# Kernel tuning notes

Hardware: AMD Instinct MI355X
Metric: run time of the kernel (lower is better)

## Reference

```python
import jax, jax.numpy as jnp
import numpy as np

CHAR_SIZE = 155   # len of the module's char_list
B, S, C, D = 64, 128, 16, 256


def setup_inputs() -> dict:
    key = jax.random.key(0)
    k1, k2, k3, k4 = jax.random.split(key, 4)
    x = jax.random.randint(k1, (B, S, C), 0, CHAR_SIZE)
    emb = jax.random.normal(k2, (CHAR_SIZE, D), dtype=jnp.float32) * 0.05
    W = jax.random.normal(k3, (D, 4 * D), dtype=jnp.float32) * 0.05
    U = jax.random.normal(k4, (D, 4 * D), dtype=jnp.float32) * 0.05
    b = jnp.zeros((4 * D,), dtype=jnp.float32)
    return {"x": x, "emb": emb, "W": W, "U": U, "b": b}


def reference(x, emb, W, U, b):
    b_, s_, c_ = x.shape
    d = emb.shape[1]
    e = emb[x]                                   # (B, S, C, D) embedding lookup
    xs = e.reshape(b_ * s_, c_, d)               # (B*S, C, D)
    # precompute input contributions for all timesteps (one big GEMM)
    xz = jnp.einsum('btd,de->bte', xs, W) + b    # (B*S, C, 4D)

    def step(carry, z_x):
        h, c = carry
        z = z_x + h @ U                          # (B*S, 4D)
        zi, zf, zg, zo = jnp.split(z, 4, axis=-1)  # Keras gate order i,f,c,o
        i = jax.nn.sigmoid(zi)
        f = jax.nn.sigmoid(zf)
        o = jax.nn.sigmoid(zo)
        c = f * c + i * zg                       # activation=None -> identity candidate
        h = o * c                                # activation=None -> identity output
        return (h, c), None

    h0 = jnp.zeros((b_ * s_, d), dtype=xz.dtype)
    (h, _), _ = jax.lax.scan(step, (h0, h0), jnp.swapaxes(xz, 0, 1))
    return h.reshape(b_, s_, d)                  # (B, S, D)
```

## Files before the change

### kernel.cpp

```cpp
#include <hip/hip_runtime.h>
#include <hip/hip_bf16.h>


#define DD      256
#define G4      1024
#define NCHAR   155
#define TSTEPS  16
#define RTILE   32
#define NROWS   8192
#define NBLOCKS (NROWS / RTILE)
#define NTHREADS 512

typedef __attribute__((ext_vector_type(8))) short bf16x8;
typedef __attribute__((ext_vector_type(8))) unsigned short u16x8;
typedef __attribute__((ext_vector_type(4))) float f32x4;

__device__ inline unsigned short f2bf_bits(float f) {
    __hip_bfloat16 h = __float2bfloat16(f);
    return *reinterpret_cast<unsigned short*>(&h);
}

__device__ inline float sigmoid_fast(float x) {
    return __builtin_amdgcn_rcpf(1.f + __expf(-x));
}

__global__ __launch_bounds__(256)
void embw_kernel(const float* __restrict__ emb, const float* __restrict__ W,
                 const float* __restrict__ b, unsigned short* __restrict__ embWp8) {
    const int i   = blockIdx.x;
    const int tid = threadIdx.x;
    float a0 = b[tid], a1 = b[256 + tid], a2 = b[512 + tid], a3 = b[768 + tid];
    const float* er = emb + i * DD;
    for (int k = 0; k < DD; ++k) {
        const float e = er[k];
        const float* wr = W + k * G4 + tid;
        a0 += e * wr[0];
        a1 += e * wr[256];
        a2 += e * wr[512];
        a3 += e * wr[768];
    }
    const int w = tid >> 5, l15 = tid & 15, nn = (tid >> 4) & 1;
    unsigned short* o = embWp8 + ((i * 8 + w) * 16 + l15) * 8 + nn;
    o[0] = f2bf_bits(a0); o[2] = f2bf_bits(a1);
    o[4] = f2bf_bits(a2); o[6] = f2bf_bits(a3);
}

__global__ __launch_bounds__(256)
void upack_kernel(const float* __restrict__ U, bf16x8* __restrict__ up) {
    const int gid  = blockIdx.x * 256 + threadIdx.x;
    const int lane = gid & 63;
    const int nt   = (gid >> 6) & 7;
    const int kt   = (gid >> 9) & 7;
    const int w    = gid >> 12;
    const int g = nt >> 1, nn = nt & 1;
    const int col = g * 256 + w * 32 + nn * 16 + (lane & 15);
    const int k0  = kt * 32 + (lane >> 4) * 8;
    bf16x8 v;
#pragma unroll
    for (int j = 0; j < 8; ++j) v[j] = (short)f2bf_bits(U[(k0 + j) * G4 + col]);
    up[gid] = v;
}


#define LOADB(DST, KT)                                                          \
    _Pragma("unroll")                                                           \
    for (int nt = 0; nt < 8; ++nt) (DST)[nt] = upw[((KT) * 8 + nt) * 64 + lane];

#define LOADB5(DST)                                                             \
    _Pragma("unroll")                                                           \
    for (int i5 = 0; i5 < 5; ++i5) (DST)[i5] = upw[(11 + i5) * 64 + lane];

#define AFR_LOAD(KT)                                                            \
        const int kb = ((KT) * 32 + lg * 8) * 2;                                \
        const int r0 = l15, r1 = 16 + l15;                                      \
        bf16x8 afr0 = *(const bf16x8*)(rbb + ((r0 * 512 + kb) ^ ((r0 & 7) << 4))); \
        bf16x8 afr1 = *(const bf16x8*)(rbb + ((r1 * 512 + kb) ^ ((r1 & 7) << 4)));

#define AFR_MFMA(KT, BARR)                                                      \
    {   AFR_LOAD(KT)                                                            \
        _Pragma("unroll")                                                       \
        for (int nt = 0; nt < 8; ++nt) {                                        \
            acc[0][nt] = __builtin_amdgcn_mfma_f32_16x16x32_bf16(               \
                afr0, (BARR)[nt], acc[0][nt], 0, 0, 0);                         \
            acc[1][nt] = __builtin_amdgcn_mfma_f32_16x16x32_bf16(               \
                afr1, (BARR)[nt], acc[1][nt], 0, 0, 0);                         \
        }                                                                       \
    }

#define AFR_LDS0()                                                              \
    {   AFR_LOAD(0)                                                             \
        const char* bp = (const char*)BresU + w * 8192 + lane * 16;             \
        _Pragma("unroll")                                                       \
        for (int nt = 0; nt < 8; ++nt) {                                        \
            bf16x8 bf = *(const bf16x8*)(bp + nt * 1024);                       \
            acc[0][nt] = __builtin_amdgcn_mfma_f32_16x16x32_bf16(               \
                afr0, bf, acc[0][nt], 0, 0, 0);                                 \
            acc[1][nt] = __builtin_amdgcn_mfma_f32_16x16x32_bf16(               \
                afr1, bf, acc[1][nt], 0, 0, 0);                                 \
        }                                                                       \
    }

#define AFR_MIX1(BARR5)                                                         \
    {   AFR_LOAD(1)                                                             \
        const char* bp = (const char*)B1resU + w * 3072 + lane * 16;            \
        _Pragma("unroll")                                                       \
        for (int nt = 0; nt < 3; ++nt) {                                        \
            bf16x8 bf = *(const bf16x8*)(bp + nt * 1024);                       \
            acc[0][nt] = __builtin_amdgcn_mfma_f32_16x16x32_bf16(               \
                afr0, bf, acc[0][nt], 0, 0, 0);                                 \
            acc[1][nt] = __builtin_amdgcn_mfma_f32_16x16x32_bf16(               \
                afr1, bf, acc[1][nt], 0, 0, 0);                                 \
        }                                                                       \
        _Pragma("unroll")                                                       \
        for (int nt = 3; nt < 8; ++nt) {                                        \
            acc[0][nt] = __builtin_amdgcn_mfma_f32_16x16x32_bf16(               \
                afr0, (BARR5)[nt - 3], acc[0][nt], 0, 0, 0);                    \
            acc[1][nt] = __builtin_amdgcn_mfma_f32_16x16x32_bf16(               \
                afr1, (BARR5)[nt - 3], acc[1][nt], 0, 0, 0);                    \
        }                                                                       \
    }

__global__ __launch_bounds__(NTHREADS)
void lstm_mfma(const int* __restrict__ x, const unsigned short* __restrict__ embWp8,
               const bf16x8* __restrict__ up, float* __restrict__ out) {
    __shared__ __align__(16) unsigned short hb[2][RTILE * DD];
    __shared__ float cb[RTILE * 257];
    __shared__ int   xs[RTILE * TSTEPS];
    __shared__ __align__(16) unsigned short BresU[8 * 8 * 64 * 8];
    __shared__ __align__(16) unsigned short B1resU[8 * 3 * 64 * 8];

    const int tid  = threadIdx.x;
    const int w    = tid >> 6;
    const int lane = tid & 63;
    const int l15  = lane & 15, lg = lane >> 4;
    const int base = blockIdx.x * RTILE;

    xs[tid] = x[base * TSTEPS + tid];

    f32x4 acc[2][8];

#pragma unroll
    for (int mt = 0; mt < 2; ++mt)
#pragma unroll
        for (int nn = 0; nn < 2; ++nn)
#pragma unroll
            for (int j = 0; j < 4; ++j)
                cb[(mt * 16 + lg * 4 + j) * 257 + w * 32 + nn * 16 + l15] = 0.f;

    const bf16x8* upw = up + w * 4096;

    {
        char* bp = (char*)BresU + w * 8192 + lane * 16;
#pragma unroll
        for (int nt = 0; nt < 8; ++nt)
            *(bf16x8*)(bp + nt * 1024) = upw[nt * 64 + lane];
        char* b1 = (char*)B1resU + w * 3072 + lane * 16;
#pragma unroll
        for (int nt = 0; nt < 3; ++nt)
            *(bf16x8*)(b1 + nt * 1024) = upw[(8 + nt) * 64 + lane];
    }

    __syncthreads();

#pragma unroll 1
    for (int t = 0; t < TSTEPS; ++t) {
#pragma unroll
        for (int mt = 0; mt < 2; ++mt) {
#pragma unroll
            for (int j = 0; j < 4; ++j) {
                const int r    = mt * 16 + lg * 4 + j;
                const int xrow = xs[r * TSTEPS + t];
                const u16x8 u =
                    *(const u16x8*)(embWp8 + ((xrow * 8 + w) * 16 + l15) * 8);
#pragma unroll
                for (int gg = 0; gg < 8; ++gg)
                    acc[mt][gg][j] = __uint_as_float((unsigned)u[gg] << 16);
            }
        }

        if (t > 0) {
            const char* rbb = (const char*)hb[(t - 1) & 1];
            bf16x8 bA[8], bB[8];
            LOADB5(bB)
            LOADB(bA, 2)
            AFR_LDS0()
            AFR_MIX1(bB)
#pragma unroll 1
            for (int ktp = 0; ktp < 3; ++ktp) {
                const int kt0 = 2 * ktp + 2, kt1 = kt0 + 1;
                LOADB(bB, kt1)
                AFR_MFMA(kt0, bA)
                if (ktp < 2) { LOADB(bA, kt0 + 2) }
                AFR_MFMA(kt1, bB)
            }
        }

        {
            char* wbb = (char*)hb[t & 1];
#pragma unroll
            for (int mt = 0; mt < 2; ++mt) {
#pragma unroll
                for (int nn = 0; nn < 2; ++nn) {
#pragma unroll
                    for (int j = 0; j < 4; ++j) {
                        const float zi = acc[mt][0 + nn][j];
                        const float zf = acc[mt][2 + nn][j];
                        const float zg = acc[mt][4 + nn][j];
                        const float zo = acc[mt][6 + nn][j];
                        const float ig = sigmoid_fast(zi);
                        const float fg = sigmoid_fast(zf);
                        const float og = sigmoid_fast(zo);
                        const int row = mt * 16 + lg * 4 + j;
                        const int d   = w * 32 + nn * 16 + l15;
                        float* cp = &cb[row * 257 + d];
                        const float cn = fg * (*cp) + ig * zg;
                        *cp = cn;
                        const float h = og * cn;
                        *(unsigned short*)(wbb +
                            ((row * 512 + d * 2) ^ ((row & 7) << 4))) = f2bf_bits(h);
                        if (t == TSTEPS - 1) out[(base + row) * DD + d] = h;
                    }
                }
            }
        }
        __syncthreads();
    }
}

extern "C" void kernel_launch(void* const* d_in, const int* in_sizes, int n_in,
                              void* d_out, int out_size, void* d_ws, size_t ws_size,
                              hipStream_t stream) {
    const int*   x   = (const int*)d_in[0];
    const float* emb = (const float*)d_in[1];
    const float* W   = (const float*)d_in[2];
    const float* U   = (const float*)d_in[3];
    const float* b   = (const float*)d_in[4];
    float* out = (float*)d_out;

    unsigned short* embWp8 = (unsigned short*)d_ws;
    bf16x8*         up     = (bf16x8*)((char*)d_ws + (1 << 20));

    embw_kernel<<<NCHAR, 256, 0, stream>>>(emb, W, b, embWp8);
    upack_kernel<<<128, 256, 0, stream>>>(U, up);
    lstm_mfma<<<NBLOCKS, NTHREADS, 0, stream>>>(x, embWp8, up, out);
}
```

Baseline: 127.4 us.

## Software-pipeline U fragment loads in half-tile chunks and store cell state as fp16

Replaces the two-stage 8-fragment B-register double buffer with a fully unrolled four-buffer rotation of 4-fragment chunks. Global loads of U fragments are issued ahead of the MFMAs that consume them, and the embedding gathers are hoisted before the accumulator init. One more kt=1 chunk of U now lives in LDS, and the cell-state scratch shrinks from fp32 to fp16 to make room. The aim is to hide global load latency inside the recurrent matmul, at the cost of register pressure and reduced cell-state precision across the 16 steps.

Measured after the change: 239.7 us. 1.88x slower.

```diff
diff --git a/kernel.cpp b/kernel.cpp
--- a/kernel.cpp
+++ b/kernel.cpp
@@ -62,33 +62,33 @@
 }
 
 
-#define LOADB(DST, KT)                                                          \
+#define LOADC(DST, CI)                                                          \
     _Pragma("unroll")                                                           \
-    for (int nt = 0; nt < 8; ++nt) (DST)[nt] = upw[((KT) * 8 + nt) * 64 + lane];
-
-#define LOADB5(DST)                                                             \
-    _Pragma("unroll")                                                           \
-    for (int i5 = 0; i5 < 5; ++i5) (DST)[i5] = upw[(11 + i5) * 64 + lane];
-
-#define AFR_LOAD(KT)                                                            \
+    for (int i4 = 0; i4 < 4; ++i4)                                              \
+        (DST)[i4] = upw[(12 + 4 * (CI) + i4) * 64 + lane];
+
+#define AFRSET(KT)                                                              \
+    {                                                                           \
         const int kb = ((KT) * 32 + lg * 8) * 2;                                \
         const int r0 = l15, r1 = 16 + l15;                                      \
-        bf16x8 afr0 = *(const bf16x8*)(rbb + ((r0 * 512 + kb) ^ ((r0 & 7) << 4))); \
-        bf16x8 afr1 = *(const bf16x8*)(rbb + ((r1 * 512 + kb) ^ ((r1 & 7) << 4)));
-
-#define AFR_MFMA(KT, BARR)                                                      \
-    {   AFR_LOAD(KT)                                                            \
+        afr0 = *(const bf16x8*)(rbb + ((r0 * 512 + kb) ^ ((r0 & 7) << 4)));     \
+        afr1 = *(const bf16x8*)(rbb + ((r1 * 512 + kb) ^ ((r1 & 7) << 4)));     \
+    }
+
+#define CONS(BUF, HALF)                                                         \
+    {                                                                           \
         _Pragma("unroll")                                                       \
-        for (int nt = 0; nt < 8; ++nt) {                                        \
+        for (int q = 0; q < 4; ++q) {                                           \
+            const int nt = (HALF) * 4 + q;                                      \
             acc[0][nt] = __builtin_amdgcn_mfma_f32_16x16x32_bf16(               \
-                afr0, (BARR)[nt], acc[0][nt], 0, 0, 0);                         \
+                afr0, (BUF)[q], acc[0][nt], 0, 0, 0);                           \
             acc[1][nt] = __builtin_amdgcn_mfma_f32_16x16x32_bf16(               \
-                afr1, (BARR)[nt], acc[1][nt], 0, 0, 0);                         \
+                afr1, (BUF)[q], acc[1][nt], 0, 0, 0);                           \
         }                                                                       \
     }
 
-#define AFR_LDS0()                                                              \
-    {   AFR_LOAD(0)                                                             \
+#define KT0_LDS()                                                               \
+    {                                                                           \
         const char* bp = (const char*)BresU + w * 8192 + lane * 16;             \
         _Pragma("unroll")                                                       \
         for (int nt = 0; nt < 8; ++nt) {                                        \
@@ -100,34 +100,27 @@
         }                                                                       \
     }
 
-#define AFR_MIX1(BARR5)                                                         \
-    {   AFR_LOAD(1)                                                             \
-        const char* bp = (const char*)B1resU + w * 3072 + lane * 16;            \
+#define KT1_LDS()                                                               \
+    {                                                                           \
+        const char* bp = (const char*)B1resU + w * 4096 + lane * 16;            \
         _Pragma("unroll")                                                       \
-        for (int nt = 0; nt < 3; ++nt) {                                        \
+        for (int nt = 0; nt < 4; ++nt) {                                        \
             bf16x8 bf = *(const bf16x8*)(bp + nt * 1024);                       \
             acc[0][nt] = __builtin_amdgcn_mfma_f32_16x16x32_bf16(               \
                 afr0, bf, acc[0][nt], 0, 0, 0);                                 \
             acc[1][nt] = __builtin_amdgcn_mfma_f32_16x16x32_bf16(               \
                 afr1, bf, acc[1][nt], 0, 0, 0);                                 \
         }                                                                       \
-        _Pragma("unroll")                                                       \
-        for (int nt = 3; nt < 8; ++nt) {                                        \
-            acc[0][nt] = __builtin_amdgcn_mfma_f32_16x16x32_bf16(               \
-                afr0, (BARR5)[nt - 3], acc[0][nt], 0, 0, 0);                    \
-            acc[1][nt] = __builtin_amdgcn_mfma_f32_16x16x32_bf16(               \
-                afr1, (BARR5)[nt - 3], acc[1][nt], 0, 0, 0);                    \
-        }                                                                       \
     }
 
 __global__ __launch_bounds__(NTHREADS)
 void lstm_mfma(const int* __restrict__ x, const unsigned short* __restrict__ embWp8,
                const bf16x8* __restrict__ up, float* __restrict__ out) {
     __shared__ __align__(16) unsigned short hb[2][RTILE * DD];
-    __shared__ float cb[RTILE * 257];
+    __shared__ unsigned short cb2[RTILE * 257];
     __shared__ int   xs[RTILE * TSTEPS];
     __shared__ __align__(16) unsigned short BresU[8 * 8 * 64 * 8];
-    __shared__ __align__(16) unsigned short B1resU[8 * 3 * 64 * 8];
+    __shared__ __align__(16) unsigned short B1resU[8 * 4 * 64 * 8];
 
     const int tid  = threadIdx.x;
     const int w    = tid >> 6;
@@ -145,7 +138,7 @@
         for (int nn = 0; nn < 2; ++nn)
 #pragma unroll
             for (int j = 0; j < 4; ++j)
-                cb[(mt * 16 + lg * 4 + j) * 257 + w * 32 + nn * 16 + l15] = 0.f;
+                cb2[(mt * 16 + lg * 4 + j) * 257 + w * 32 + nn * 16 + l15] = 0;
 
     const bf16x8* upw = up + w * 4096;
 
@@ -154,9 +147,9 @@
 #pragma unroll
         for (int nt = 0; nt < 8; ++nt)
             *(bf16x8*)(bp + nt * 1024) = upw[nt * 64 + lane];
-        char* b1 = (char*)B1resU + w * 3072 + lane * 16;
-#pragma unroll
-        for (int nt = 0; nt < 3; ++nt)
+        char* b1 = (char*)B1resU + w * 4096 + lane * 16;
+#pragma unroll
+        for (int nt = 0; nt < 4; ++nt)
             *(bf16x8*)(b1 + nt * 1024) = upw[(8 + nt) * 64 + lane];
     }
 
@@ -164,35 +157,46 @@
 
 #pragma unroll 1
     for (int t = 0; t < TSTEPS; ++t) {
-#pragma unroll
-        for (int mt = 0; mt < 2; ++mt) {
+        u16x8 gv[2][4];
+#pragma unroll
+        for (int mt = 0; mt < 2; ++mt)
 #pragma unroll
             for (int j = 0; j < 4; ++j) {
                 const int r    = mt * 16 + lg * 4 + j;
                 const int xrow = xs[r * TSTEPS + t];
-                const u16x8 u =
+                gv[mt][j] =
                     *(const u16x8*)(embWp8 + ((xrow * 8 + w) * 16 + l15) * 8);
+            }
+
+        bf16x8 A4[4], B4[4], C4[4], D4[4];
+        bf16x8 afr0, afr1;
+        if (t > 0) { LOADC(A4, 0) LOADC(B4, 1) LOADC(C4, 2) }
+
+#pragma unroll
+        for (int mt = 0; mt < 2; ++mt)
+#pragma unroll
+            for (int j = 0; j < 4; ++j)
 #pragma unroll
                 for (int gg = 0; gg < 8; ++gg)
-                    acc[mt][gg][j] = __uint_as_float((unsigned)u[gg] << 16);
-            }
-        }
+                    acc[mt][gg][j] = __uint_as_float((unsigned)gv[mt][j][gg] << 16);
 
         if (t > 0) {
             const char* rbb = (const char*)hb[(t - 1) & 1];
-            bf16x8 bA[8], bB[8];
-            LOADB5(bB)
-            LOADB(bA, 2)
-            AFR_LDS0()
-            AFR_MIX1(bB)
-#pragma unroll 1
-            for (int ktp = 0; ktp < 3; ++ktp) {
-                const int kt0 = 2 * ktp + 2, kt1 = kt0 + 1;
-                LOADB(bB, kt1)
-                AFR_MFMA(kt0, bA)
-                if (ktp < 2) { LOADB(bA, kt0 + 2) }
-                AFR_MFMA(kt1, bB)
-            }
+            AFRSET(0) KT0_LDS()
+            AFRSET(1) KT1_LDS()
+            LOADC(D4, 3)   CONS(A4, 1)
+            AFRSET(2) LOADC(A4, 4)  CONS(B4, 0)
+                      LOADC(B4, 5)  CONS(C4, 1)
+            AFRSET(3) LOADC(C4, 6)  CONS(D4, 0)
+                      LOADC(D4, 7)  CONS(A4, 1)
+            AFRSET(4) LOADC(A4, 8)  CONS(B4, 0)
+                      LOADC(B4, 9)  CONS(C4, 1)
+            AFRSET(5) LOADC(C4, 10) CONS(D4, 0)
+                      LOADC(D4, 11) CONS(A4, 1)
+            AFRSET(6) LOADC(A4, 12) CONS(B4, 0)
+                                    CONS(C4, 1)
+            AFRSET(7)               CONS(D4, 0)
+                                    CONS(A4, 1)
         }
 
         {
@@ -212,9 +216,9 @@
                         const float og = sigmoid_fast(zo);
                         const int row = mt * 16 + lg * 4 + j;
                         const int d   = w * 32 + nn * 16 + l15;
-                        float* cp = &cb[row * 257 + d];
-                        const float cn = fg * (*cp) + ig * zg;
-                        *cp = cn;
+                        _Float16* cp = (_Float16*)&cb2[row * 257 + d];
+                        const float cn = fg * (float)(*cp) + ig * zg;
+                        *cp = (_Float16)cn;
                         const float h = og * cn;
                         *(unsigned short*)(wbb +
                             ((row * 512 + d * 2) ^ ((row & 7) << 4))) = f2bf_bits(h);
```

## Keep cell state in fp16 registers, single h buffer, cache two U k-tiles in LDS

Applied to the files above, without the earlier changes.

Moves the LSTM cell state out of shared memory into a per-thread fp16 register vector, and replaces the double-buffered h tile with a single buffer guarded by an extra barrier per step. It also widens the second LDS-resident slice of U to a full k-tile, so the first two k-tiles come from LDS and the rest stream from global. This cuts LDS traffic and footprint but adds a __syncthreads per timestep, and storing c in fp16 loses precision compared with fp32.

Result: faster. 113.5 us, median of 2 (-10.8%).

```diff
diff --git a/kernel.cpp b/kernel.cpp
--- a/kernel.cpp
+++ b/kernel.cpp
@@ -14,6 +14,7 @@
 typedef __attribute__((ext_vector_type(8))) short bf16x8;
 typedef __attribute__((ext_vector_type(8))) unsigned short u16x8;
 typedef __attribute__((ext_vector_type(4))) float f32x4;
+typedef __attribute__((ext_vector_type(16))) _Float16 f16x16;
 
 __device__ inline unsigned short f2bf_bits(float f) {
     __hip_bfloat16 h = __float2bfloat16(f);
@@ -66,10 +67,6 @@
     _Pragma("unroll")                                                           \
     for (int nt = 0; nt < 8; ++nt) (DST)[nt] = upw[((KT) * 8 + nt) * 64 + lane];
 
-#define LOADB5(DST)                                                             \
-    _Pragma("unroll")                                                           \
-    for (int i5 = 0; i5 < 5; ++i5) (DST)[i5] = upw[(11 + i5) * 64 + lane];
-
 #define AFR_LOAD(KT)                                                            \
         const int kb = ((KT) * 32 + lg * 8) * 2;                                \
         const int r0 = l15, r1 = 16 + l15;                                      \
@@ -87,9 +84,9 @@
         }                                                                       \
     }
 
-#define AFR_LDS0()                                                              \
-    {   AFR_LOAD(0)                                                             \
-        const char* bp = (const char*)BresU + w * 8192 + lane * 16;             \
+#define AFR_LDSRES(KT, BASE)                                                    \
+    {   AFR_LOAD(KT)                                                            \
+        const char* bp = (const char*)(BASE) + w * 8192 + lane * 16;            \
         _Pragma("unroll")                                                       \
         for (int nt = 0; nt < 8; ++nt) {                                        \
             bf16x8 bf = *(const bf16x8*)(bp + nt * 1024);                       \
@@ -100,34 +97,13 @@
         }                                                                       \
     }
 
-#define AFR_MIX1(BARR5)                                                         \
-    {   AFR_LOAD(1)                                                             \
-        const char* bp = (const char*)B1resU + w * 3072 + lane * 16;            \
-        _Pragma("unroll")                                                       \
-        for (int nt = 0; nt < 3; ++nt) {                                        \
-            bf16x8 bf = *(const bf16x8*)(bp + nt * 1024);                       \
-            acc[0][nt] = __builtin_amdgcn_mfma_f32_16x16x32_bf16(               \
-                afr0, bf, acc[0][nt], 0, 0, 0);                                 \
-            acc[1][nt] = __builtin_amdgcn_mfma_f32_16x16x32_bf16(               \
-                afr1, bf, acc[1][nt], 0, 0, 0);                                 \
-        }                                                                       \
-        _Pragma("unroll")                                                       \
-        for (int nt = 3; nt < 8; ++nt) {                                        \
-            acc[0][nt] = __builtin_amdgcn_mfma_f32_16x16x32_bf16(               \
-                afr0, (BARR5)[nt - 3], acc[0][nt], 0, 0, 0);                    \
-            acc[1][nt] = __builtin_amdgcn_mfma_f32_16x16x32_bf16(               \
-                afr1, (BARR5)[nt - 3], acc[1][nt], 0, 0, 0);                    \
-        }                                                                       \
-    }
-
 __global__ __launch_bounds__(NTHREADS)
 void lstm_mfma(const int* __restrict__ x, const unsigned short* __restrict__ embWp8,
                const bf16x8* __restrict__ up, float* __restrict__ out) {
-    __shared__ __align__(16) unsigned short hb[2][RTILE * DD];
-    __shared__ float cb[RTILE * 257];
-    __shared__ int   xs[RTILE * TSTEPS];
+    __shared__ __align__(16) unsigned short hb[RTILE * DD];
+    __shared__ int xs[RTILE * TSTEPS];
     __shared__ __align__(16) unsigned short BresU[8 * 8 * 64 * 8];
-    __shared__ __align__(16) unsigned short B1resU[8 * 3 * 64 * 8];
+    __shared__ __align__(16) unsigned short B1resU[8 * 8 * 64 * 8];
 
     const int tid  = threadIdx.x;
     const int w    = tid >> 6;
@@ -138,14 +114,9 @@
     xs[tid] = x[base * TSTEPS + tid];
 
     f32x4 acc[2][8];
-
-#pragma unroll
-    for (int mt = 0; mt < 2; ++mt)
-#pragma unroll
-        for (int nn = 0; nn < 2; ++nn)
-#pragma unroll
-            for (int j = 0; j < 4; ++j)
-                cb[(mt * 16 + lg * 4 + j) * 257 + w * 32 + nn * 16 + l15] = 0.f;
+    f16x16 cst;
+#pragma unroll
+    for (int i = 0; i < 16; ++i) cst[i] = (_Float16)0.f;
 
     const bf16x8* upw = up + w * 4096;
 
@@ -154,9 +125,9 @@
 #pragma unroll
         for (int nt = 0; nt < 8; ++nt)
             *(bf16x8*)(bp + nt * 1024) = upw[nt * 64 + lane];
-        char* b1 = (char*)B1resU + w * 3072 + lane * 16;
-#pragma unroll
-        for (int nt = 0; nt < 3; ++nt)
+        char* b1 = (char*)B1resU + w * 8192 + lane * 16;
+#pragma unroll
+        for (int nt = 0; nt < 8; ++nt)
             *(bf16x8*)(b1 + nt * 1024) = upw[(8 + nt) * 64 + lane];
     }
 
@@ -179,24 +150,25 @@
         }
 
         if (t > 0) {
-            const char* rbb = (const char*)hb[(t - 1) & 1];
+            const char* rbb = (const char*)hb;
             bf16x8 bA[8], bB[8];
-            LOADB5(bB)
-            LOADB(bA, 2)
-            AFR_LDS0()
-            AFR_MIX1(bB)
+            LOADB(bA, 2) LOADB(bB, 3)
+            AFR_LDSRES(0, BresU)
+            AFR_LDSRES(1, B1resU)
 #pragma unroll 1
             for (int ktp = 0; ktp < 3; ++ktp) {
-                const int kt0 = 2 * ktp + 2, kt1 = kt0 + 1;
-                LOADB(bB, kt1)
-                AFR_MFMA(kt0, bA)
-                if (ktp < 2) { LOADB(bA, kt0 + 2) }
-                AFR_MFMA(kt1, bB)
+                const int kta = 2 * ktp + 2, ktb = kta + 1;
+                AFR_MFMA(kta, bA)
+                if (ktp < 2) { LOADB(bA, kta + 2) }
+                AFR_MFMA(ktb, bB)
+                if (ktp < 2) { LOADB(bB, ktb + 2) }
             }
         }
 
+        __syncthreads();
+
         {
-            char* wbb = (char*)hb[t & 1];
+            char* wbb = (char*)hb;
 #pragma unroll
             for (int mt = 0; mt < 2; ++mt) {
 #pragma unroll
@@ -210,12 +182,12 @@
                         const float ig = sigmoid_fast(zi);
                         const float fg = sigmoid_fast(zf);
                         const float og = sigmoid_fast(zo);
+                        const int ci = mt * 8 + nn * 4 + j;
+                        const float cn = fg * (float)cst[ci] + ig * zg;
+                        cst[ci] = (_Float16)cn;
+                        const float h = og * cn;
                         const int row = mt * 16 + lg * 4 + j;
                         const int d   = w * 32 + nn * 16 + l15;
-                        float* cp = &cb[row * 257 + d];
-                        const float cn = fg * (*cp) + ig * zg;
-                        *cp = cn;
-                        const float h = og * cn;
                         *(unsigned short*)(wbb +
                             ((row * 512 + d * 2) ^ ((row & 7) << 4))) = f2bf_bits(h);
                         if (t == TSTEPS - 1) out[(base + row) * DD + d] = h;
```
